# Kernel optimization log

Hardware: AMD Instinct MI355X
Metric: run time of the kernel (lower is better)

The kernel has to match this reference:

```python
import jax, jax.numpy as jnp
import numpy as np

N, E, D_IN, HID, D_OUT = 200000, 5000000, 128, 16, 2


def setup_inputs() -> dict:
    key = jax.random.key(0)
    ks = jax.random.split(key, 8)
    x = jax.random.normal(ks[0], (N, D_IN), dtype=jnp.float32)
    edge_index = jax.random.randint(ks[1], (2, E), 0, N, dtype=jnp.int32)
    W1 = jax.random.normal(ks[2], (D_IN, HID), dtype=jnp.float32) / np.sqrt(D_IN)
    b1 = jnp.zeros((HID,), dtype=jnp.float32)
    W3 = jax.random.normal(ks[3], (HID, HID), dtype=jnp.float32) / np.sqrt(HID)
    b3 = jnp.zeros((HID,), dtype=jnp.float32)
    W2 = jax.random.normal(ks[4], (HID, D_OUT), dtype=jnp.float32) / np.sqrt(HID)
    b2 = jnp.zeros((D_OUT,), dtype=jnp.float32)
    return {"x": x, "edge_index": edge_index, "W1": W1, "b1": b1,
            "W3": W3, "b3": b3, "W2": W2, "b2": b2}


def reference(x, edge_index, W1, b1, W3, b3, W2, b2):
    # GCNConv: add self-loops, symmetric normalization, aggregate, linear+bias.
    src, dst = edge_index[0], edge_index[1]
    loops = jnp.arange(N, dtype=src.dtype)
    src_f = jnp.concatenate([src, loops])  # [E+N]
    dst_f = jnp.concatenate([dst, loops])
    deg = jax.ops.segment_sum(jnp.ones_like(src_f, dtype=jnp.float32), dst_f,
                              num_segments=N)
    dis = jnp.where(deg > 0, jax.lax.rsqrt(jnp.maximum(deg, 1.0)), 0.0)
    norm = dis[src_f] * dis[dst_f]  # [E+N]

    def gcn_conv(h, W, b):
        h = h @ W                                   # [N, F_out] small GEMM
        msg = h[src_f] * norm[:, None]              # gather + scale
        agg = jax.ops.segment_sum(msg, dst_f, num_segments=N)  # scatter-add
        return agg + b

    h = jax.nn.relu(gcn_conv(x, W1, b1))    # conv1 (dropout is identity in eval)
    h = jax.nn.relu(gcn_conv(h, W3, b3))    # conv3 loop (conv_number-2 = 1 iter)
    h = gcn_conv(h, W2, b2)                 # conv2
    return jax.nn.log_softmax(h, axis=1)
```

## Files before the change

### kernel.cpp

```cpp
#include <hip/hip_runtime.h>

#define NN 200000
#define NE 5000000
#define DIN 128
#define HID 16
#define DOUT 2
#define BSZ 391
#define NB 512
#define LBITS 9
#define NCH 8
#define SLICE_DIV 25000
#define NK (NB * NCH)
#define NKB 512
#define SKEYS 4096
#define PB 512
#define PT 512

static_assert((size_t)NB * BSZ >= NN, "bucket coverage");
static_assert((NN - 1) / SLICE_DIV == NCH - 1, "slice count");
static_assert(NE % 4 == 0, "int4 edge reads");


__global__ __launch_bounds__(PT) void hist_pass(const int4* __restrict__ dst4,
                                                int* __restrict__ blockHist) {
    __shared__ int h[NKB];
    for (int k = threadIdx.x; k < NKB; k += PT) h[k] = 0;
    __syncthreads();
    const int NI = NE / 4;
    for (int i = blockIdx.x * PT + threadIdx.x; i < NI; i += PB * PT) {
        int4 d = dst4[i];
        atomicAdd(&h[d.x / BSZ], 1);
        atomicAdd(&h[d.y / BSZ], 1);
        atomicAdd(&h[d.z / BSZ], 1);
        atomicAdd(&h[d.w / BSZ], 1);
    }
    __syncthreads();
    for (int k = threadIdx.x; k < NKB; k += PT)
        blockHist[(size_t)blockIdx.x * NKB + k] = h[k];
}

__global__ __launch_bounds__(256) void tot_pass(const int* __restrict__ blockHist,
                                                int* __restrict__ chunkStart) {
    int k = blockIdx.x * 256 + threadIdx.x;
    if (k >= NKB) return;
    int s = 0;
#pragma unroll 16
    for (int b = 0; b < PB; ++b) s += blockHist[(size_t)b * NKB + k];
    chunkStart[k] = s;
}

__global__ __launch_bounds__(NKB) void scan_keys(int* __restrict__ chunkStart) {
    __shared__ int wsum[8];
    int t = threadIdx.x;
    int lane = t & 63, w = t >> 6;
    int v = chunkStart[t];
    int inc = v;
    for (int off = 1; off < 64; off <<= 1) {
        int nb = __shfl_up(inc, off, 64);
        if (lane >= off) inc += nb;
    }
    if (lane == 63) wsum[w] = inc;
    __syncthreads();
    if (t == 0) {
        int car = 0;
#pragma unroll
        for (int i = 0; i < 8; ++i) { int u = wsum[i]; wsum[i] = car; car += u; }
    }
    __syncthreads();
    chunkStart[t] = inc - v + wsum[w];
    if (t == 0) chunkStart[NKB] = NE;
}

__global__ __launch_bounds__(256) void offsets_pass(int* __restrict__ blockHist,
                                                    const int* __restrict__ chunkStart) {
    int k = blockIdx.x * 256 + threadIdx.x;
    if (k >= NKB) return;
    int r = chunkStart[k];
#pragma unroll 8
    for (int b = 0; b < PB; ++b) {
        size_t idx = (size_t)b * NKB + k;
        int v = blockHist[idx];
        blockHist[idx] = r;
        r += v;
    }
}

__global__ __launch_bounds__(PT) void scatter_pass(const int4* __restrict__ src4,
                                                   const int4* __restrict__ dst4,
                                                   const int* __restrict__ blockHist,
                                                   unsigned* __restrict__ pedge) {
    __shared__ int cur[NKB];
    for (int k = threadIdx.x; k < NKB; k += PT)
        cur[k] = blockHist[(size_t)blockIdx.x * NKB + k];
    __syncthreads();
    const int NI = NE / 4;
    for (int i = blockIdx.x * PT + threadIdx.x; i < NI; i += PB * PT) {
        int4 s = src4[i];
        int4 d = dst4[i];
        int b0 = d.x / BSZ, b1 = d.y / BSZ, b2 = d.z / BSZ, b3 = d.w / BSZ;
        int p0 = atomicAdd(&cur[b0], 1);
        int p1 = atomicAdd(&cur[b1], 1);
        int p2 = atomicAdd(&cur[b2], 1);
        int p3 = atomicAdd(&cur[b3], 1);
        pedge[p0] = ((unsigned)s.x << LBITS) | (unsigned)(d.x - b0 * BSZ);
        pedge[p1] = ((unsigned)s.y << LBITS) | (unsigned)(d.y - b1 * BSZ);
        pedge[p2] = ((unsigned)s.z << LBITS) | (unsigned)(d.z - b2 * BSZ);
        pedge[p3] = ((unsigned)s.w << LBITS) | (unsigned)(d.w - b3 * BSZ);
    }
}


__global__ __launch_bounds__(512) void subsort(const unsigned* __restrict__ pedge,
                                               const int* __restrict__ chunkStart,
                                               int* __restrict__ pedge2,
                                               int* __restrict__ rowStart,
                                               float* __restrict__ dis) {
    __shared__ int h[SKEYS];
    __shared__ int wsum[8];
    int t = threadIdx.x;
    int b = blockIdx.x;
    int lane = t & 63, w = t >> 6;
    int e0 = chunkStart[b], e1 = chunkStart[b + 1];
    for (int k = t; k < SKEYS; k += 512) h[k] = 0;
    __syncthreads();
    for (int i = e0 + t; i < e1; i += 512) {
        unsigned p = pedge[i];
        int sv = (int)(p >> LBITS);
        atomicAdd(&h[(sv / SLICE_DIV) * 512 + (p & 511u)], 1);
    }
    __syncthreads();
    if (t < BSZ) {
        int dg = 1;
#pragma unroll
        for (int s = 0; s < NCH; ++s) dg += h[s * 512 + t];
        int node = b * BSZ + t;
        if (node < NN) dis[node] = rsqrtf((float)dg);
    }
    int vals[8];
    int s = 0;
#pragma unroll
    for (int j = 0; j < 8; ++j) { vals[j] = h[t * 8 + j]; s += vals[j]; }
    int inc = s;
    for (int off = 1; off < 64; off <<= 1) {
        int nb = __shfl_up(inc, off, 64);
        if (lane >= off) inc += nb;
    }
    if (lane == 63) wsum[w] = inc;
    __syncthreads();
    if (t == 0) {
        int car = 0;
#pragma unroll
        for (int i = 0; i < 8; ++i) { int u = wsum[i]; wsum[i] = car; car += u; }
    }
    __syncthreads();
    int run = inc - s + wsum[w];
#pragma unroll
    for (int j = 0; j < 8; ++j) {
        int k = t * 8 + j;
        h[k] = run;
        int dl = k & 511, sl = k >> 9;
        if (dl < BSZ)
            rowStart[(size_t)(b * NCH + sl) * BSZ + dl] = e0 + run;
        run += vals[j];
    }
    __syncthreads();
    for (int i = e0 + t; i < e1; i += 512) {
        unsigned p = pedge[i];
        int sv = (int)(p >> LBITS);
        int key = (sv / SLICE_DIV) * 512 + (p & 511u);
        int pos = atomicAdd(&h[key], 1);
        pedge2[e0 + pos] = sv;
    }
    if (b == 0 && t == 0) rowStart[(size_t)NK * BSZ] = NE;
}


#define GXT 512
#define GXR 128
__global__ __launch_bounds__(GXT) void gemm_x_w1(const float* __restrict__ x,
                                                 const float* __restrict__ W,
                                                 const float* __restrict__ dis,
                                                 float* __restrict__ out) {
    __shared__ float w[DIN * HID];
    int t = threadIdx.x;
    for (int i = t; i < DIN * HID; i += GXT) w[i] = W[i];
    __syncthreads();
    int row = blockIdx.x * GXR + (t >> 2);
    int c0 = (t & 3) * 4;
    if (row >= NN) return;
    const float4* xr = reinterpret_cast<const float4*>(x + (size_t)row * DIN);
    float ax = 0.f, ay = 0.f, az = 0.f, aw = 0.f;
#pragma unroll
    for (int k4 = 0; k4 < DIN / 4; ++k4) {
        float4 xv = xr[k4];
        float4 w0 = *reinterpret_cast<const float4*>(&w[(4 * k4 + 0) * HID + c0]);
        float4 w1 = *reinterpret_cast<const float4*>(&w[(4 * k4 + 1) * HID + c0]);
        float4 w2 = *reinterpret_cast<const float4*>(&w[(4 * k4 + 2) * HID + c0]);
        float4 w3 = *reinterpret_cast<const float4*>(&w[(4 * k4 + 3) * HID + c0]);
        ax += xv.x * w0.x + xv.y * w1.x + xv.z * w2.x + xv.w * w3.x;
        ay += xv.x * w0.y + xv.y * w1.y + xv.z * w2.y + xv.w * w3.y;
        az += xv.x * w0.z + xv.y * w1.z + xv.z * w2.z + xv.w * w3.z;
        aw += xv.x * w0.w + xv.y * w1.w + xv.z * w2.w + xv.w * w3.w;
    }
    float dd = dis[row];
    *reinterpret_cast<float4*>(&out[(size_t)row * HID + c0]) =
        make_float4(ax * dd, ay * dd, az * dd, aw * dd);
}

__global__ __launch_bounds__(256) void gemm_h_w16(const float* __restrict__ h,
                                                  const float* __restrict__ W,
                                                  const float* __restrict__ dis,
                                                  float* __restrict__ out) {
    __shared__ float w[HID * HID];
    if (threadIdx.x < HID * HID) w[threadIdx.x] = W[threadIdx.x];
    __syncthreads();
    int row = blockIdx.x * 16 + (threadIdx.x >> 4);
    int c = threadIdx.x & 15;
    if (row >= NN) return;
    const float4* hr = reinterpret_cast<const float4*>(h + (size_t)row * HID);
    float acc = 0.f;
#pragma unroll
    for (int k4 = 0; k4 < HID / 4; ++k4) {
        float4 v = hr[k4];
        acc += v.x * w[(4 * k4 + 0) * HID + c] + v.y * w[(4 * k4 + 1) * HID + c]
             + v.z * w[(4 * k4 + 2) * HID + c] + v.w * w[(4 * k4 + 3) * HID + c];
    }
    out[row * HID + c] = acc * dis[row];
}

__global__ __launch_bounds__(256) void gemm_h_w2(const float* __restrict__ h,
                                                 const float* __restrict__ W,
                                                 const float* __restrict__ dis,
                                                 float* __restrict__ out) {
    int t = blockIdx.x * 256 + threadIdx.x;
    int row = t >> 1;
    int c = t & 1;
    if (row >= NN) return;
    const float* hr = h + (size_t)row * HID;
    float acc = 0.f;
#pragma unroll
    for (int k = 0; k < HID; ++k) acc += hr[k] * W[k * DOUT + c];
    out[row * DOUT + c] = acc * dis[row];
}


__device__ __forceinline__ void acc_edges(const int* __restrict__ pedge2,
                                          const float4* __restrict__ xs4,
                                          int e, int e1, int c4, float4& a) {
    for (; e + 3 < e1; e += 4) {
        int s0 = pedge2[e], s1 = pedge2[e + 1];
        int s2 = pedge2[e + 2], s3 = pedge2[e + 3];
        float4 u0 = xs4[(s0 << 2) + c4];
        float4 u1 = xs4[(s1 << 2) + c4];
        float4 u2 = xs4[(s2 << 2) + c4];
        float4 u3 = xs4[(s3 << 2) + c4];
        a.x += (u0.x + u1.x) + (u2.x + u3.x);
        a.y += (u0.y + u1.y) + (u2.y + u3.y);
        a.z += (u0.z + u1.z) + (u2.z + u3.z);
        a.w += (u0.w + u1.w) + (u2.w + u3.w);
    }
    for (; e < e1; ++e) {
        float4 u = xs4[(pedge2[e] << 2) + c4];
        a.x += u.x; a.y += u.y; a.z += u.z; a.w += u.w;
    }
}

__global__ __launch_bounds__(1024, 8) void agg16_all(const int* __restrict__ pedge2,
                                                     const int* __restrict__ rowStart,
                                                     const float* __restrict__ xs,
                                                     const float* __restrict__ dis,
                                                     const float* __restrict__ bias,
                                                     float* __restrict__ buf,
                                                     int relu) {
    int t = threadIdx.x;
    int b = blockIdx.x;
    int base = b * BSZ;
    int c4 = t & 3;
    int q = t >> 2;
    int g0 = (q * BSZ) >> 8;
    int g1 = ((q + 1) * BSZ) >> 8;
    bool two = (g1 - g0) == 2;
    int n0 = base + g0, n1 = base + g0 + 1;
    bool v0 = n0 < NN;
    bool v1 = two && (n1 < NN);
    const float4* xs4 = reinterpret_cast<const float4*>(xs);
    float4* buf4 = reinterpret_cast<float4*>(buf);
    float4 a0 = make_float4(0.f, 0.f, 0.f, 0.f);
    float4 a1 = a0;
    if (v0) a0 = xs4[(n0 << 2) + c4];
    if (v1) a1 = xs4[(n1 << 2) + c4];
    for (int r = 0; r < NCH; ++r) {
        const int* rs = rowStart + (size_t)(b * NCH + r) * BSZ;
        if (v0) acc_edges(pedge2, xs4, rs[g0], rs[g0 + 1], c4, a0);
        if (v1) acc_edges(pedge2, xs4, rs[g0 + 1], rs[g0 + 2], c4, a1);
    }
    float4 bb = reinterpret_cast<const float4*>(bias)[c4];
    if (v0) {
        float dd = dis[n0];
        float4 v = make_float4(dd * a0.x + bb.x, dd * a0.y + bb.y,
                               dd * a0.z + bb.z, dd * a0.w + bb.w);
        if (relu) { v.x = fmaxf(v.x, 0.f); v.y = fmaxf(v.y, 0.f);
                    v.z = fmaxf(v.z, 0.f); v.w = fmaxf(v.w, 0.f); }
        buf4[(n0 << 2) + c4] = v;
    }
    if (v1) {
        float dd = dis[n1];
        float4 v = make_float4(dd * a1.x + bb.x, dd * a1.y + bb.y,
                               dd * a1.z + bb.z, dd * a1.w + bb.w);
        if (relu) { v.x = fmaxf(v.x, 0.f); v.y = fmaxf(v.y, 0.f);
                    v.z = fmaxf(v.z, 0.f); v.w = fmaxf(v.w, 0.f); }
        buf4[(n1 << 2) + c4] = v;
    }
}

__global__ __launch_bounds__(512) void agg2_lsm(const int* __restrict__ pedge2,
                                                const int* __restrict__ rowStart,
                                                const float* __restrict__ xs,
                                                const float* __restrict__ dis,
                                                const float* __restrict__ bias,
                                                float* __restrict__ out) {
    int t = threadIdx.x;
    int b = blockIdx.x;
    if (t >= BSZ) return;
    int node = b * BSZ + t;
    if (node >= NN) return;
    const float2* xs2 = reinterpret_cast<const float2*>(xs);
    float a0 = 0.f, a1 = 0.f;
    for (int s = 0; s < NCH; ++s) {
        const int* rs = rowStart + (size_t)(b * NCH + s) * BSZ;
        int e = rs[t], e1 = rs[t + 1];
        for (; e + 3 < e1; e += 4) {
            int s0 = pedge2[e], s1 = pedge2[e + 1];
            int s2 = pedge2[e + 2], s3 = pedge2[e + 3];
            float2 v0 = xs2[s0], v1 = xs2[s1], v2 = xs2[s2], v3 = xs2[s3];
            a0 += (v0.x + v1.x) + (v2.x + v3.x);
            a1 += (v0.y + v1.y) + (v2.y + v3.y);
        }
        for (; e < e1; ++e) {
            float2 v = xs2[pedge2[e]];
            a0 += v.x; a1 += v.y;
        }
    }
    float2 sv = xs2[node];
    float d = dis[node];
    float v0 = (a0 + sv.x) * d + bias[0];
    float v1 = (a1 + sv.y) * d + bias[1];
    float m = fmaxf(v0, v1);
    float lse = m + logf(__expf(v0 - m) + __expf(v1 - m));
    reinterpret_cast<float2*>(out)[node] = make_float2(v0 - lse, v1 - lse);
}


extern "C" void kernel_launch(void* const* d_in, const int* in_sizes, int n_in,
                              void* d_out, int out_size, void* d_ws, size_t ws_size,
                              hipStream_t stream) {
    const float* x = (const float*)d_in[0];
    const int* ei = (const int*)d_in[1];
    const float* W1 = (const float*)d_in[2];
    const float* b1 = (const float*)d_in[3];
    const float* W3 = (const float*)d_in[4];
    const float* b3 = (const float*)d_in[5];
    const float* W2 = (const float*)d_in[6];
    const float* b2 = (const float*)d_in[7];
    float* out = (float*)d_out;

    const int4* src4 = (const int4*)ei;
    const int4* dst4 = (const int4*)(ei + NE);

    int* W = (int*)d_ws;
    unsigned* pedge = (unsigned*)W;
    int* pedge2 = W + NE;
    int* rowStart = W + 2 * (size_t)NE;
    int* blockHist = rowStart + (size_t)NK * BSZ + 4;
    int* chunkStart = blockHist + (size_t)PB * NKB;
    float* dis = (float*)(chunkStart + NKB + 4);
    float* bufB = dis + NN;
    float* bufA = (float*)W;

    const int B = 256;
    auto cdiv = [](long long a, long long b) { return (int)((a + b - 1) / b); };

    hist_pass<<<PB, PT, 0, stream>>>(dst4, blockHist);
    tot_pass<<<cdiv(NKB, 256), 256, 0, stream>>>(blockHist, chunkStart);
    scan_keys<<<1, NKB, 0, stream>>>(chunkStart);
    offsets_pass<<<cdiv(NKB, 256), 256, 0, stream>>>(blockHist, chunkStart);
    scatter_pass<<<PB, PT, 0, stream>>>(src4, dst4, blockHist, pedge);
    subsort<<<NB, 512, 0, stream>>>(pedge, chunkStart, pedge2, rowStart, dis);

    gemm_x_w1<<<cdiv(NN, GXR), GXT, 0, stream>>>(x, W1, dis, bufA);
    agg16_all<<<NB, 1024, 0, stream>>>(pedge2, rowStart, bufA, dis, b1, bufB, 1);

    gemm_h_w16<<<cdiv(NN, 16), B, 0, stream>>>(bufB, W3, dis, bufA);
    agg16_all<<<NB, 1024, 0, stream>>>(pedge2, rowStart, bufA, dis, b3, bufB, 1);

    gemm_h_w2<<<cdiv((long long)NN * DOUT, B), B, 0, stream>>>(bufB, W2, dis, bufA);
    agg2_lsm<<<NB, 512, 0, stream>>>(pedge2, rowStart, bufA, dis, b2, out);
}
```

Measured before the change: 301.9 us.

## Reorder subsort keys node-major to build a single per-node CSR rowStart

The subsort histogram key changes from slice-major to node-major (local dst × 8 + source slice). Each node's edges are now contiguous, still ordered by source slice, and rowStart becomes a plain per-node CSR array instead of eight per-slice tables. Degree is taken from the per-thread key sum, and the aggregation kernels read one edge range per node instead of looping over eight slices, which removes rowStart loads and loop overhead. The trade-off is that nodes within a block no longer sweep source slices in lockstep, which may weaken L2 locality of the gathered features.

```diff
diff --git a/kernel.cpp b/kernel.cpp
--- a/kernel.cpp
+++ b/kernel.cpp
@@ -10,7 +10,6 @@
 #define LBITS 9
 #define NCH 8
 #define SLICE_DIV 25000
-#define NK (NB * NCH)
 #define NKB 512
 #define SKEYS 4096
 #define PB 512
@@ -126,20 +125,17 @@
     for (int i = e0 + t; i < e1; i += 512) {
         unsigned p = pedge[i];
         int sv = (int)(p >> LBITS);
-        atomicAdd(&h[(sv / SLICE_DIV) * 512 + (p & 511u)], 1);
-    }
-    __syncthreads();
-    if (t < BSZ) {
-        int dg = 1;
-#pragma unroll
-        for (int s = 0; s < NCH; ++s) dg += h[s * 512 + t];
-        int node = b * BSZ + t;
-        if (node < NN) dis[node] = rsqrtf((float)dg);
-    }
+        atomicAdd(&h[((p & 511u) << 3) + sv / SLICE_DIV], 1);
+    }
+    __syncthreads();
     int vals[8];
     int s = 0;
 #pragma unroll
     for (int j = 0; j < 8; ++j) { vals[j] = h[t * 8 + j]; s += vals[j]; }
+    {
+        int node = b * BSZ + t;
+        if (t < BSZ && node < NN) dis[node] = rsqrtf((float)(s + 1));
+    }
     int inc = s;
     for (int off = 1; off < 64; off <<= 1) {
         int nb = __shfl_up(inc, off, 64);
@@ -154,24 +150,20 @@
     }
     __syncthreads();
     int run = inc - s + wsum[w];
+    if (t < BSZ) rowStart[b * BSZ + t] = e0 + run;
 #pragma unroll
     for (int j = 0; j < 8; ++j) {
-        int k = t * 8 + j;
-        h[k] = run;
-        int dl = k & 511, sl = k >> 9;
-        if (dl < BSZ)
-            rowStart[(size_t)(b * NCH + sl) * BSZ + dl] = e0 + run;
+        h[t * 8 + j] = run;
         run += vals[j];
     }
     __syncthreads();
     for (int i = e0 + t; i < e1; i += 512) {
         unsigned p = pedge[i];
         int sv = (int)(p >> LBITS);
-        int key = (sv / SLICE_DIV) * 512 + (p & 511u);
+        int key = ((p & 511u) << 3) + sv / SLICE_DIV;
         int pos = atomicAdd(&h[key], 1);
         pedge2[e0 + pos] = sv;
     }
-    if (b == 0 && t == 0) rowStart[(size_t)NK * BSZ] = NE;
 }
 
 
@@ -289,10 +281,13 @@
     float4 a1 = a0;
     if (v0) a0 = xs4[(n0 << 2) + c4];
     if (v1) a1 = xs4[(n1 << 2) + c4];
-    for (int r = 0; r < NCH; ++r) {
-        const int* rs = rowStart + (size_t)(b * NCH + r) * BSZ;
-        if (v0) acc_edges(pedge2, xs4, rs[g0], rs[g0 + 1], c4, a0);
-        if (v1) acc_edges(pedge2, xs4, rs[g0 + 1], rs[g0 + 2], c4, a1);
+    if (v0) {
+        int ea = rowStart[n0], eb = rowStart[n0 + 1];
+        acc_edges(pedge2, xs4, ea, eb, c4, a0);
+        if (v1) {
+            int ec = rowStart[n1 + 1];
+            acc_edges(pedge2, xs4, eb, ec, c4, a1);
+        }
     }
     float4 bb = reinterpret_cast<const float4*>(bias)[c4];
     if (v0) {
@@ -326,20 +321,17 @@
     if (node >= NN) return;
     const float2* xs2 = reinterpret_cast<const float2*>(xs);
     float a0 = 0.f, a1 = 0.f;
-    for (int s = 0; s < NCH; ++s) {
-        const int* rs = rowStart + (size_t)(b * NCH + s) * BSZ;
-        int e = rs[t], e1 = rs[t + 1];
-        for (; e + 3 < e1; e += 4) {
-            int s0 = pedge2[e], s1 = pedge2[e + 1];
-            int s2 = pedge2[e + 2], s3 = pedge2[e + 3];
-            float2 v0 = xs2[s0], v1 = xs2[s1], v2 = xs2[s2], v3 = xs2[s3];
-            a0 += (v0.x + v1.x) + (v2.x + v3.x);
-            a1 += (v0.y + v1.y) + (v2.y + v3.y);
-        }
-        for (; e < e1; ++e) {
-            float2 v = xs2[pedge2[e]];
-            a0 += v.x; a1 += v.y;
-        }
+    int e = rowStart[node], e1 = rowStart[node + 1];
+    for (; e + 3 < e1; e += 4) {
+        int s0 = pedge2[e], s1 = pedge2[e + 1];
+        int s2 = pedge2[e + 2], s3 = pedge2[e + 3];
+        float2 v0 = xs2[s0], v1 = xs2[s1], v2 = xs2[s2], v3 = xs2[s3];
+        a0 += (v0.x + v1.x) + (v2.x + v3.x);
+        a1 += (v0.y + v1.y) + (v2.y + v3.y);
+    }
+    for (; e < e1; ++e) {
+        float2 v = xs2[pedge2[e]];
+        a0 += v.x; a1 += v.y;
     }
     float2 sv = xs2[node];
     float d = dis[node];
@@ -371,7 +363,7 @@
     unsigned* pedge = (unsigned*)W;
     int* pedge2 = W + NE;
     int* rowStart = W + 2 * (size_t)NE;
-    int* blockHist = rowStart + (size_t)NK * BSZ + 4;
+    int* blockHist = rowStart + (size_t)NB * BSZ + 4;
     int* chunkStart = blockHist + (size_t)PB * NKB;
     float* dis = (float*)(chunkStart + NKB + 4);
     float* bufB = dis + NN;
```

New measurement: 356.2 us. +18.0%, slower.
